# Performance work log

Hardware: AMD Instinct MI355X
Metric: run time of the kernel (lower is better)

## Reference

```python
import jax, jax.numpy as jnp
import numpy as np

D_MODEL = 1024
NUM_HEADS = 16
D_K = D_MODEL // NUM_HEADS
B, T = 2, 2048


def setup_inputs() -> dict:
    key = jax.random.key(0)
    ks = jax.random.split(key, 11)
    s = 1.0 / np.sqrt(D_MODEL)
    inp = {
        "q": jax.random.normal(ks[0], (B, T, D_MODEL), jnp.float32),
        "k": jax.random.normal(ks[1], (B, T, D_MODEL), jnp.float32),
        "v": jax.random.normal(ks[2], (B, T, D_MODEL), jnp.float32),
        "mask": jnp.tril(jnp.ones((1, 1, T, T), jnp.int32)),  # causal
        "wq": jax.random.normal(ks[3], (D_MODEL, D_MODEL), jnp.float32) * s,
        "bq": jnp.zeros((D_MODEL,), jnp.float32),
        "wk": jax.random.normal(ks[4], (D_MODEL, D_MODEL), jnp.float32) * s,
        "bk": jnp.zeros((D_MODEL,), jnp.float32),
        "wv": jax.random.normal(ks[5], (D_MODEL, D_MODEL), jnp.float32) * s,
        "bv": jnp.zeros((D_MODEL,), jnp.float32),
        "wo": jax.random.normal(ks[6], (D_MODEL, D_MODEL), jnp.float32) * s,
        "bo": jnp.zeros((D_MODEL,), jnp.float32),
    }
    return inp


def reference(q, k, v, mask, wq, bq, wk, bk, wv, bv, wo, bo):
    Bq, Tq, _ = q.shape
    Tk = k.shape[1]
    # projections, split into heads: (B, H, T, d_k)
    qh = (q @ wq + bq).reshape(Bq, Tq, NUM_HEADS, D_K).transpose(0, 2, 1, 3)
    kh = (k @ wk + bk).reshape(Bq, Tk, NUM_HEADS, D_K).transpose(0, 2, 1, 3)
    vh = (v @ wv + bv).reshape(Bq, Tk, NUM_HEADS, D_K).transpose(0, 2, 1, 3)
    scores = jnp.einsum("bhqd,bhkd->bhqk", qh, kh) / jnp.sqrt(jnp.float32(D_K))
    scores = jnp.where(mask == 0, jnp.float32(-1e9), scores)
    attn = jax.nn.softmax(scores, axis=-1)
    ctx = jnp.einsum("bhqk,bhkd->bhqd", attn, vh)
    ctx = ctx.transpose(0, 2, 1, 3).reshape(Bq, Tq, D_MODEL)
    return ctx @ wo + bo
```

## Files before the change

kernel.cpp:

```cpp
#include <hip/hip_runtime.h>
#include <hip/hip_bf16.h>

#define DM 1024
#define NH 16
#define DK 64
#define TT 2048
#define BATCH 2

typedef __attribute__((ext_vector_type(8))) short bf16x8;
typedef __attribute__((ext_vector_type(4))) float f32x4;
typedef __attribute__((ext_vector_type(4))) unsigned short u16x4;
typedef unsigned short u16;

__device__ inline u16 f2b(float x){ __hip_bfloat16 h = __float2bfloat16(x); return *reinterpret_cast<u16*>(&h); }

__device__ inline void gl_lds16(const u16* g, u16* l) {
  __builtin_amdgcn_global_load_lds(
      (const __attribute__((address_space(1))) unsigned int*)g,
      (__attribute__((address_space(3))) unsigned int*)l, 16, 0, 0);
}

__global__ __launch_bounds__(256) void prep(const float* __restrict__ q, const float* __restrict__ k,
                                            const float* __restrict__ v,
                                            const float* __restrict__ wq, const float* __restrict__ wk,
                                            const float* __restrict__ wv, const float* __restrict__ wo,
                                            u16* __restrict__ qb, u16* __restrict__ kb,
                                            u16* __restrict__ vb, u16* __restrict__ wt) {
  int z = blockIdx.z;
  if (z < 3) {
    const float* src = z==0 ? q : z==1 ? k : v;
    u16* dst = z==0 ? qb : z==1 ? kb : vb;
    size_t i = ((size_t)blockIdx.x*256 + threadIdx.x)*8;
    f32x4 a = *(const f32x4*)(src+i);
    f32x4 b = *(const f32x4*)(src+i+4);
    union { bf16x8 v8; u16 e[8]; } u;
    #pragma unroll
    for (int j=0;j<4;j++){ u.e[j] = f2b(a[j]); u.e[4+j] = f2b(b[j]); }
    *(bf16x8*)(dst+i) = u.v8;
  } else {
    int bx = blockIdx.x;
    if (bx >= 1024) return;
    __shared__ float tile[32][33];
    const float* src = z==3 ? wq : z==4 ? wk : z==5 ? wv : wo;
    u16* dst = wt + (size_t)(z-3)*DM*DM;
    int bxx = bx & 31, byy = bx >> 5;
    int tx = threadIdx.x & 31, ty = threadIdx.x >> 5;
    int x  = bxx*32 + tx;
    int y0 = byy*32 + ty;
    #pragma unroll
    for (int i=0;i<32;i+=8) tile[ty+i][tx] = src[(size_t)(y0+i)*DM + x];
    __syncthreads();
    int xo = byy*32 + tx;
    int yo = bxx*32 + ty;
    #pragma unroll
    for (int i=0;i<32;i+=8) dst[(size_t)(yo+i)*DM + xo] = f2b(tile[tx][ty+i]);
  }
}

__global__ __launch_bounds__(256) void gemm_qkv(const u16* __restrict__ qb, const u16* __restrict__ kb,
                                                const u16* __restrict__ vb, const u16* __restrict__ wt,
                                                const float* __restrict__ bq, const float* __restrict__ bk,
                                                const float* __restrict__ bv,
                                                u16* __restrict__ qh, u16* __restrict__ kh,
                                                u16* __restrict__ vhT) {
  const int z = blockIdx.z;
  const u16* A = z==0 ? qb : z==1 ? kb : vb;
  const u16* W = wt + (size_t)z*DM*DM;
  const float* bias = z==0 ? bq : z==1 ? bk : bv;
  u16* outv = z==0 ? qh : z==1 ? kh : vhT;
  const int mode = (z==2) ? 1 : 0;
  const float oscale = (z==0) ? 0.125f : 1.0f;

  __shared__ __align__(16) u16 As[3][128*32];
  __shared__ __align__(16) u16 Bs[3][128*32];
  const int tid = threadIdx.x, lane = tid & 63, wid = tid >> 6;
  const int li = lane & 15, quad = lane >> 4;
  const int row0 = blockIdx.x*128, col0 = blockIdx.y*128;
  const int wr = wid & 1, wc = wid >> 1;

  const int srow = lane >> 2;
  const int scol = ((lane & 3) ^ ((srow >> 1) & 3)) * 8;
  const int rsw  = (li >> 1) & 3;

  auto stage = [&](int hh, int bufi) {
    const int kk = hh*32;
    #pragma unroll
    for (int c=0;c<2;c++) {
      int ch = wid*2 + c;
      gl_lds16(A + (size_t)(row0 + ch*16 + srow)*DM + kk + scol, &As[bufi][ch*512]);
      gl_lds16(W + (size_t)(col0 + ch*16 + srow)*DM + kk + scol, &Bs[bufi][ch*512]);
    }
  };

  f32x4 acc[4][4];
  #pragma unroll
  for (int i=0;i<4;i++)
    #pragma unroll
    for (int j=0;j<4;j++) acc[i][j] = f32x4{0.f,0.f,0.f,0.f};

  stage(0, 0);
  stage(1, 1);
  asm volatile("s_waitcnt vmcnt(4)" ::: "memory");
  __builtin_amdgcn_s_barrier();

  int buf = 0;
  for (int h = 0; h < 32; h++) {
    bf16x8 a[4], b[4];
    #pragma unroll
    for (int i=0;i<4;i++) a[i] = *(const bf16x8*)&As[buf][(wr*64 + i*16 + li)*32 + (quad ^ rsw)*8];
    #pragma unroll
    for (int j=0;j<4;j++) b[j] = *(const bf16x8*)&Bs[buf][(wc*64 + j*16 + li)*32 + (quad ^ rsw)*8];

    if (h < 30) { int nb = buf + 2; if (nb >= 3) nb -= 3; stage(h+2, nb); }

    __builtin_amdgcn_s_setprio(1);
    #pragma unroll
    for (int i=0;i<4;i++)
      #pragma unroll
      for (int j=0;j<4;j++)
        acc[i][j] = __builtin_amdgcn_mfma_f32_16x16x32_bf16(a[i], b[j], acc[i][j], 0,0,0);
    __builtin_amdgcn_s_setprio(0);

    if (h < 30)       asm volatile("s_waitcnt vmcnt(4)" ::: "memory");
    else if (h == 30) asm volatile("s_waitcnt vmcnt(0)" ::: "memory");
    __builtin_amdgcn_s_barrier();
    if (++buf == 3) buf = 0;
  }

  if (mode == 0) {
    #pragma unroll
    for (int j=0;j<4;j++) {
      int col = col0 + wc*64 + j*16 + li;
      float bsv = bias[col];
      #pragma unroll
      for (int i=0;i<4;i++) {
        int rowb = row0 + wr*64 + i*16 + quad*4;
        #pragma unroll
        for (int r=0;r<4;r++)
          outv[(size_t)(rowb + r)*DM + col] = f2b((acc[i][j][r] + bsv) * oscale);
      }
    }
  } else {
    #pragma unroll
    for (int j=0;j<4;j++) {
      int col = col0 + wc*64 + j*16 + li;
      float bsv = bias[col];
      int hh = col >> 6, d = col & 63;
      #pragma unroll
      for (int i=0;i<4;i++) {
        int rowb = row0 + wr*64 + i*16 + quad*4;
        int bb = rowb >> 11, t0 = rowb & (TT-1);
        u16x4 w;
        #pragma unroll
        for (int r=0;r<4;r++) w[r] = f2b(acc[i][j][r] + bsv);
        *(u16x4*)&outv[(((size_t)(bb*NH + hh)*DK + d)*TT) + t0] = w;
      }
    }
  }
}

__global__ __launch_bounds__(256) void gemm_out64(const u16* __restrict__ A, const u16* __restrict__ W,
                                                  const float* __restrict__ bias, float* __restrict__ out) {
  __shared__ __align__(16) u16 As[3][128*32];
  __shared__ __align__(16) u16 Bs[3][64*32];
  const int tid = threadIdx.x, lane = tid & 63, wid = tid >> 6;
  const int li = lane & 15, quad = lane >> 4;
  const int row0 = blockIdx.x*128, col0 = blockIdx.y*64;
  const int wr = wid & 1, wc = wid >> 1;

  const int srow = lane >> 2;
  const int scol = ((lane & 3) ^ ((srow >> 1) & 3)) * 8;
  const int rsw  = (li >> 1) & 3;

  auto stage = [&](int hh, int bufi) {
    const int kk = hh*32;
    #pragma unroll
    for (int c=0;c<2;c++) {
      int ch = wid*2 + c;
      gl_lds16(A + (size_t)(row0 + ch*16 + srow)*DM + kk + scol, &As[bufi][ch*512]);
    }
    gl_lds16(W + (size_t)(col0 + wid*16 + srow)*DM + kk + scol, &Bs[bufi][wid*512]);
  };

  f32x4 acc[4][2];
  #pragma unroll
  for (int i=0;i<4;i++)
    #pragma unroll
    for (int j=0;j<2;j++) acc[i][j] = f32x4{0.f,0.f,0.f,0.f};

  stage(0, 0);
  stage(1, 1);
  asm volatile("s_waitcnt vmcnt(3)" ::: "memory");
  __builtin_amdgcn_s_barrier();

  int buf = 0;
  for (int h = 0; h < 32; h++) {
    bf16x8 a[4], b[2];
    #pragma unroll
    for (int i=0;i<4;i++) a[i] = *(const bf16x8*)&As[buf][(wr*64 + i*16 + li)*32 + (quad ^ rsw)*8];
    #pragma unroll
    for (int j=0;j<2;j++) b[j] = *(const bf16x8*)&Bs[buf][(wc*32 + j*16 + li)*32 + (quad ^ rsw)*8];

    if (h < 30) { int nb = buf + 2; if (nb >= 3) nb -= 3; stage(h+2, nb); }

    __builtin_amdgcn_s_setprio(1);
    #pragma unroll
    for (int i=0;i<4;i++)
      #pragma unroll
      for (int j=0;j<2;j++)
        acc[i][j] = __builtin_amdgcn_mfma_f32_16x16x32_bf16(a[i], b[j], acc[i][j], 0,0,0);
    __builtin_amdgcn_s_setprio(0);

    if (h < 30)       asm volatile("s_waitcnt vmcnt(3)" ::: "memory");
    else if (h == 30) asm volatile("s_waitcnt vmcnt(0)" ::: "memory");
    __builtin_amdgcn_s_barrier();
    if (++buf == 3) buf = 0;
  }

  #pragma unroll
  for (int j=0;j<2;j++) {
    int col = col0 + wc*32 + j*16 + li;
    float bsv = bias[col];
    #pragma unroll
    for (int i=0;i<4;i++) {
      #pragma unroll
      for (int r=0;r<4;r++) {
        int row = row0 + wr*64 + i*16 + quad*4 + r;
        out[(size_t)row*DM + col] = acc[i][j][r] + bsv;
      }
    }
  }
}

__global__ __launch_bounds__(256) void flash(const u16* __restrict__ qh, const u16* __restrict__ kh,
                                             const u16* __restrict__ vhT, u16* __restrict__ ctx) {
  const int bh = blockIdx.x;
  const int pr = blockIdx.y;
  const int b = bh >> 4, h = bh & 15;
  const u16* Q  = qh  + (size_t)b*TT*DM + h*DK;
  const u16* K  = kh  + (size_t)b*TT*DM + h*DK;
  const u16* Vt = vhT + (size_t)bh*DK*TT;

  const int tid = threadIdx.x, lane = tid & 63, wid = tid >> 6;
  const int li = lane & 15, quad = lane >> 4;

  __shared__ u16 Kl[64][72];
  __shared__ u16 Vl[64][72];
  __shared__ u16 Pb[4][16][72];

  const int sr = tid >> 3;
  const int sc = (tid & 7) * 8;

  bf16x8 kr0 = *(const bf16x8*)&K[(size_t)(sr   )*DM + sc];
  bf16x8 kr1 = *(const bf16x8*)&K[(size_t)(sr+32)*DM + sc];
  bf16x8 vr0 = *(const bf16x8*)&Vt[(size_t)(sr   )*TT + sc];
  bf16x8 vr1 = *(const bf16x8*)&Vt[(size_t)(sr+32)*TT + sc];

  #pragma unroll
  for (int ph = 0; ph < 2; ph++) {
    const int qt = (ph == 0) ? pr : (31 - pr);
    const int nt = qt + 1;
    const int qrow0 = qt*64 + wid*16;

    bf16x8 qf0 = *(const bf16x8*)&Q[(size_t)(qrow0+li)*DM +      quad*8];
    bf16x8 qf1 = *(const bf16x8*)&Q[(size_t)(qrow0+li)*DM + 32 + quad*8];

    f32x4 o[4];
    #pragma unroll
    for (int d=0;d<4;d++) o[d] = f32x4{0.f,0.f,0.f,0.f};
    float lp = 0.f;

    for (int it = 0; it < nt; it++) {
      const int k0 = it*64;
      __syncthreads();
      *(bf16x8*)&Kl[sr   ][sc] = kr0;
      *(bf16x8*)&Kl[sr+32][sc] = kr1;
      *(bf16x8*)&Vl[sr   ][sc] = vr0;
      *(bf16x8*)&Vl[sr+32][sc] = vr1;
      __syncthreads();
      if (it+1 < nt) {
        const int k1 = k0 + 64;
        kr0 = *(const bf16x8*)&K[(size_t)(k1+sr   )*DM + sc];
        kr1 = *(const bf16x8*)&K[(size_t)(k1+sr+32)*DM + sc];
        vr0 = *(const bf16x8*)&Vt[(size_t)(sr   )*TT + k1 + sc];
        vr1 = *(const bf16x8*)&Vt[(size_t)(sr+32)*TT + k1 + sc];
      } else if (ph == 0) {
        kr0 = *(const bf16x8*)&K[(size_t)(sr   )*DM + sc];
        kr1 = *(const bf16x8*)&K[(size_t)(sr+32)*DM + sc];
        vr0 = *(const bf16x8*)&Vt[(size_t)(sr   )*TT + sc];
        vr1 = *(const bf16x8*)&Vt[(size_t)(sr+32)*TT + sc];
      }

      f32x4 s[4];
      #pragma unroll
      for (int c=0;c<4;c++) {
        bf16x8 kf0 = *(const bf16x8*)&Kl[c*16+li][     quad*8];
        bf16x8 kf1 = *(const bf16x8*)&Kl[c*16+li][32 + quad*8];
        f32x4 t = __builtin_amdgcn_mfma_f32_16x16x32_bf16(kf0, qf0, f32x4{0.f,0.f,0.f,0.f}, 0,0,0);
        s[c]    = __builtin_amdgcn_mfma_f32_16x16x32_bf16(kf1, qf1, t, 0,0,0);
      }
      const bool dg = (it == nt-1);
      const int qq = qrow0 + li;
      float p[4][4];
      if (dg) {
        #pragma unroll
        for (int c=0;c<4;c++)
          #pragma unroll
          for (int r=0;r<4;r++){
            int key = k0 + c*16 + quad*4 + r;
            p[c][r] = (key <= qq) ? __expf(s[c][r]) : 0.f;
          }
      } else {
        #pragma unroll
        for (int c=0;c<4;c++)
          #pragma unroll
          for (int r=0;r<4;r++)
            p[c][r] = __expf(s[c][r]);
      }
      #pragma unroll
      for (int c=0;c<4;c++)
        #pragma unroll
        for (int r=0;r<4;r++)
          lp += p[c][r];

      #pragma unroll
      for (int c=0;c<4;c++) {
        u16x4 w;
        #pragma unroll
        for (int r=0;r<4;r++) w[r] = f2b(p[c][r]);
        *(u16x4*)&Pb[wid][li][c*16 + quad*4] = w;
      }
      __builtin_amdgcn_wave_barrier();
      __asm__ __volatile__("s_waitcnt lgkmcnt(0)");
      bf16x8 pf0 = *(const bf16x8*)&Pb[wid][li][     quad*8];
      bf16x8 pf1 = *(const bf16x8*)&Pb[wid][li][32 + quad*8];

      #pragma unroll
      for (int d=0;d<4;d++){
        bf16x8 vf0 = *(const bf16x8*)&Vl[d*16+li][     quad*8];
        bf16x8 vf1 = *(const bf16x8*)&Vl[d*16+li][32 + quad*8];
        o[d] = __builtin_amdgcn_mfma_f32_16x16x32_bf16(vf0, pf0, o[d], 0,0,0);
        o[d] = __builtin_amdgcn_mfma_f32_16x16x32_bf16(vf1, pf1, o[d], 0,0,0);
      }
    }

    lp += __shfl_xor(lp, 16, 64);
    lp += __shfl_xor(lp, 32, 64);
    float rl = 1.0f / lp;

    const int qq = qrow0 + li;
    #pragma unroll
    for (int d=0;d<4;d++){
      u16x4 w;
      #pragma unroll
      for (int r=0;r<4;r++) w[r] = f2b(o[d][r] * rl);
      *(u16x4*)&ctx[(size_t)(b*TT + qq)*DM + h*DK + d*16 + quad*4] = w;
    }
  }
}

extern "C" void kernel_launch(void* const* d_in, const int* in_sizes, int n_in,
                              void* d_out, int out_size, void* d_ws, size_t ws_size,
                              hipStream_t stream) {
  const float* q   = (const float*)d_in[0];
  const float* k   = (const float*)d_in[1];
  const float* v   = (const float*)d_in[2];
  const float* wq  = (const float*)d_in[4];
  const float* bq  = (const float*)d_in[5];
  const float* wk  = (const float*)d_in[6];
  const float* bk  = (const float*)d_in[7];
  const float* wv  = (const float*)d_in[8];
  const float* bv  = (const float*)d_in[9];
  const float* wo  = (const float*)d_in[10];
  const float* bo  = (const float*)d_in[11];
  float* out = (float*)d_out;

  const size_t SZ = (size_t)BATCH*TT*DM;
  u16* wt  = (u16*)d_ws;
  u16* qb  = wt + (size_t)4*DM*DM;
  u16* kb  = qb + SZ;
  u16* vb  = kb + SZ;
  u16* qh  = vb + SZ;
  u16* kh  = qh + SZ;
  u16* vhT = kh + SZ;
  u16* ctx = qb;

  prep<<<dim3(2048, 1, 7), 256, 0, stream>>>(q, k, v, wq, wk, wv, wo, qb, kb, vb, wt);

  gemm_qkv<<<dim3(4096/128, DM/128, 3), 256, 0, stream>>>(qb, kb, vb, wt, bq, bk, bv, qh, kh, vhT);

  flash<<<dim3(BATCH*NH, 16), 256, 0, stream>>>(qh, kh, vhT, ctx);

  gemm_out64<<<dim3(4096/128, DM/64), 256, 0, stream>>>(ctx, wt + (size_t)3*DM*DM, bo, out);
}
```

Before: 224.6 us.

## Rewrite QKV GEMM with 256x256 tiles, 512 threads, and swizzled block mapping

```diff
diff --git a/kernel.cpp b/kernel.cpp
--- a/kernel.cpp
+++ b/kernel.cpp
@@ -57,102 +57,144 @@
   }
 }
 
-__global__ __launch_bounds__(256) void gemm_qkv(const u16* __restrict__ qb, const u16* __restrict__ kb,
-                                                const u16* __restrict__ vb, const u16* __restrict__ wt,
-                                                const float* __restrict__ bq, const float* __restrict__ bk,
-                                                const float* __restrict__ bv,
-                                                u16* __restrict__ qh, u16* __restrict__ kh,
-                                                u16* __restrict__ vhT) {
-  const int z = blockIdx.z;
+__global__ __launch_bounds__(512, 2) void gemm_qkv(const u16* __restrict__ qb, const u16* __restrict__ kb,
+                                                   const u16* __restrict__ vb, const u16* __restrict__ wt,
+                                                   const float* __restrict__ bq, const float* __restrict__ bk,
+                                                   const float* __restrict__ bv,
+                                                   u16* __restrict__ qh, u16* __restrict__ kh,
+                                                   u16* __restrict__ vhT) {
+  const int bid = blockIdx.x;
+  const int swz = (bid & 7)*24 + (bid >> 3);
+  const int z  = swz >> 6;
+  const int rb = swz & 63;
+  const int row0 = (rb >> 2) * 256;
+  const int col0 = (rb & 3) * 256;
+
   const u16* A = z==0 ? qb : z==1 ? kb : vb;
   const u16* W = wt + (size_t)z*DM*DM;
   const float* bias = z==0 ? bq : z==1 ? bk : bv;
   u16* outv = z==0 ? qh : z==1 ? kh : vhT;
-  const int mode = (z==2) ? 1 : 0;
+  const int mode = (z==2);
   const float oscale = (z==0) ? 0.125f : 1.0f;
 
-  __shared__ __align__(16) u16 As[3][128*32];
-  __shared__ __align__(16) u16 Bs[3][128*32];
+  __shared__ __align__(16) u16 As[2][16384];
+  __shared__ __align__(16) u16 Bs[2][16384];
+
   const int tid = threadIdx.x, lane = tid & 63, wid = tid >> 6;
-  const int li = lane & 15, quad = lane >> 4;
-  const int row0 = blockIdx.x*128, col0 = blockIdx.y*128;
-  const int wr = wid & 1, wc = wid >> 1;
-
-  const int srow = lane >> 2;
-  const int scol = ((lane & 3) ^ ((srow >> 1) & 3)) * 8;
-  const int rsw  = (li >> 1) & 3;
-
-  auto stage = [&](int hh, int bufi) {
-    const int kk = hh*32;
-    #pragma unroll
-    for (int c=0;c<2;c++) {
-      int ch = wid*2 + c;
-      gl_lds16(A + (size_t)(row0 + ch*16 + srow)*DM + kk + scol, &As[bufi][ch*512]);
-      gl_lds16(W + (size_t)(col0 + ch*16 + srow)*DM + kk + scol, &Bs[bufi][ch*512]);
+  const int li = lane & 15, quad = lane >> 4, l7 = lane & 7;
+  const int wr = wid >> 2, wc = wid & 3;
+
+  int r_[2], gs_[2];
+  #pragma unroll
+  for (int c=0;c<2;c++){ int idx = tid + c*512; int rr = idx>>3; int gd = idx&7; r_[c]=rr; gs_[c]=gd^(rr&7); }
+
+  auto stage = [&](int op, int t, int hf, int slot){
+    const u16* base = op ? W : A;
+    const int rowbase = (op ? col0 : row0) + hf*128;
+    u16* lb = (op ? Bs[slot] : As[slot]) + hf*8192;
+    #pragma unroll
+    for (int c=0;c<2;c++){
+      gl_lds16(base + (size_t)(rowbase + r_[c])*DM + t*64 + gs_[c]*8,
+               lb + ((wid*64 + c*512) << 3));
     }
   };
 
-  f32x4 acc[4][4];
+  f32x4 acc[8][4];
   #pragma unroll
-  for (int i=0;i<4;i++)
+  for (int i=0;i<8;i++)
     #pragma unroll
     for (int j=0;j<4;j++) acc[i][j] = f32x4{0.f,0.f,0.f,0.f};
 
-  stage(0, 0);
-  stage(1, 1);
+  stage(1, 0, 0, 0); stage(1, 0, 1, 0);
+  stage(0, 0, 0, 0); stage(0, 0, 1, 0);
+  stage(1, 1, 0, 1); stage(1, 1, 1, 1);
   asm volatile("s_waitcnt vmcnt(4)" ::: "memory");
   __builtin_amdgcn_s_barrier();
 
-  int buf = 0;
-  for (int h = 0; h < 32; h++) {
-    bf16x8 a[4], b[4];
-    #pragma unroll
-    for (int i=0;i<4;i++) a[i] = *(const bf16x8*)&As[buf][(wr*64 + i*16 + li)*32 + (quad ^ rsw)*8];
-    #pragma unroll
-    for (int j=0;j<4;j++) b[j] = *(const bf16x8*)&Bs[buf][(wc*64 + j*16 + li)*32 + (quad ^ rsw)*8];
-
-    if (h < 30) { int nb = buf + 2; if (nb >= 3) nb -= 3; stage(h+2, nb); }
-
-    __builtin_amdgcn_s_setprio(1);
-    #pragma unroll
-    for (int i=0;i<4;i++)
-      #pragma unroll
-      for (int j=0;j<4;j++)
-        acc[i][j] = __builtin_amdgcn_mfma_f32_16x16x32_bf16(a[i], b[j], acc[i][j], 0,0,0);
-    __builtin_amdgcn_s_setprio(0);
-
-    if (h < 30)       asm volatile("s_waitcnt vmcnt(4)" ::: "memory");
-    else if (h == 30) asm volatile("s_waitcnt vmcnt(0)" ::: "memory");
-    __builtin_amdgcn_s_barrier();
-    if (++buf == 3) buf = 0;
-  }
-
-  if (mode == 0) {
-    #pragma unroll
-    for (int j=0;j<4;j++) {
-      int col = col0 + wc*64 + j*16 + li;
+  bf16x8 b[4][2];
+  for (int i = 0; i < 8; i++) {
+    const int t2 = 2*i;
+    #pragma unroll
+    for (int half = 0; half < 2; half++) {
+      const int slot = half;
+      #pragma unroll
+      for (int q = 0; q < 4; q++) {
+        if (q == 0) {
+          const u16* bb = Bs[slot] + (wc>>1)*8192 + (wc&1)*4096;
+          #pragma unroll
+          for (int c=0;c<4;c++)
+            #pragma unroll
+            for (int kh=0;kh<2;kh++)
+              b[c][kh] = *(const bf16x8*)&bb[(c*16 + li)*64 + ((quad + 4*kh) ^ l7)*8];
+        }
+        bf16x8 a[2][2];
+        {
+          const u16* ab = As[slot] + wr*8192;
+          #pragma unroll
+          for (int rr2=0; rr2<2; rr2++)
+            #pragma unroll
+            for (int kh=0;kh<2;kh++)
+              a[rr2][kh] = *(const bf16x8*)&ab[((q*2+rr2)*16 + li)*64 + ((quad + 4*kh) ^ l7)*8];
+        }
+        {
+          const int sop = (q >= 2);
+          const int st  = t2 + 1 + half + (q >= 2);
+          const int shf = q & 1;
+          const int ssl = (q >= 2) ? half : (1 - half);
+          if (st <= 15) stage(sop, st, shf, ssl);
+        }
+        if (q == 0) asm volatile("s_waitcnt lgkmcnt(8)" ::: "memory");
+        __builtin_amdgcn_s_barrier();
+        asm volatile("s_waitcnt lgkmcnt(0)" ::: "memory");
+        __builtin_amdgcn_sched_barrier(0);
+        __builtin_amdgcn_s_setprio(1);
+        #pragma unroll
+        for (int rr2=0; rr2<2; rr2++)
+          #pragma unroll
+          for (int c=0;c<4;c++)
+            #pragma unroll
+            for (int kh=0;kh<2;kh++)
+              acc[q*2+rr2][c] = __builtin_amdgcn_mfma_f32_16x16x32_bf16(a[rr2][kh], b[c][kh], acc[q*2+rr2][c], 0,0,0);
+        __builtin_amdgcn_s_setprio(0);
+        if (q == 3) {
+          if (half == 0) {
+            if (i < 7) asm volatile("s_waitcnt vmcnt(4)" ::: "memory");
+            else       asm volatile("s_waitcnt vmcnt(0)" ::: "memory");
+          } else {
+            if (i < 7) asm volatile("s_waitcnt vmcnt(4)" ::: "memory");
+          }
+        }
+        __builtin_amdgcn_s_barrier();
+      }
+    }
+  }
+
+  if (!mode) {
+    #pragma unroll
+    for (int c=0;c<4;c++) {
+      int col = col0 + wc*64 + c*16 + li;
       float bsv = bias[col];
       #pragma unroll
-      for (int i=0;i<4;i++) {
-        int rowb = row0 + wr*64 + i*16 + quad*4;
+      for (int fr=0; fr<8; fr++) {
+        int rowb = row0 + wr*128 + fr*16 + quad*4;
         #pragma unroll
         for (int r=0;r<4;r++)
-          outv[(size_t)(rowb + r)*DM + col] = f2b((acc[i][j][r] + bsv) * oscale);
+          outv[(size_t)(rowb + r)*DM + col] = f2b((acc[fr][c][r] + bsv) * oscale);
       }
     }
   } else {
     #pragma unroll
-    for (int j=0;j<4;j++) {
-      int col = col0 + wc*64 + j*16 + li;
+    for (int c=0;c<4;c++) {
+      int col = col0 + wc*64 + c*16 + li;
       float bsv = bias[col];
       int hh = col >> 6, d = col & 63;
       #pragma unroll
-      for (int i=0;i<4;i++) {
-        int rowb = row0 + wr*64 + i*16 + quad*4;
+      for (int fr=0; fr<8; fr++) {
+        int rowb = row0 + wr*128 + fr*16 + quad*4;
         int bb = rowb >> 11, t0 = rowb & (TT-1);
         u16x4 w;
         #pragma unroll
-        for (int r=0;r<4;r++) w[r] = f2b(acc[i][j][r] + bsv);
+        for (int r=0;r<4;r++) w[r] = f2b(acc[fr][c][r] + bsv);
         *(u16x4*)&outv[(((size_t)(bb*NH + hh)*DK + d)*TT) + t0] = w;
       }
     }
@@ -387,7 +429,7 @@
 
   prep<<<dim3(2048, 1, 7), 256, 0, stream>>>(q, k, v, wq, wk, wv, wo, qb, kb, vb, wt);
 
-  gemm_qkv<<<dim3(4096/128, DM/128, 3), 256, 0, stream>>>(qb, kb, vb, wt, bq, bk, bv, qh, kh, vhT);
+  gemm_qkv<<<dim3(192, 1, 1), 512, 0, stream>>>(qb, kb, vb, wt, bq, bk, bv, qh, kh, vhT);
 
   flash<<<dim3(BATCH*NH, 16), 256, 0, stream>>>(qh, kh, vhT, ctx);
 
```

Result: no change. 222.3 us (-1.0%).
